# Kernel optimization log

Measured on AMD Instinct MI355X. Metric: run time of the kernel, lower is better.

## Reference

```python
import jax, jax.numpy as jnp
from jax import lax
import numpy as np

K = 256   # kernel_size == hidden channels (Haar basis size)
S = 16    # stride
BN_EPS = 1e-5


def _haar_matrix_unnorm(n):
    if n == 2:
        return np.array([[1.0, 1.0], [1.0, -1.0]])
    prev = _haar_matrix_unnorm(n // 2)
    top = np.kron(prev, np.array([1.0, 1.0]))
    bot = np.kron(np.eye(n // 2), np.array([1.0, -1.0]))
    return np.concatenate((top, bot))


def haar_matrix(n):
    h = _haar_matrix_unnorm(n)
    return h / np.linalg.norm(h, axis=1, keepdims=True)


def setup_inputs() -> dict:
    key = jax.random.key(0)
    ks = jax.random.split(key, 8)
    B, T = 64, 32768
    haar = jnp.asarray(haar_matrix(K), dtype=jnp.float32)          # [K, K]
    x = jax.random.normal(ks[0], (B, 1, T), dtype=jnp.float32)
    return {
        "x": x,
        # BitwiseConv1d(1, K, K, stride=S, padding=K)
        "conv_w": haar[:, None, :],                                 # [K, 1, K] (OIH)
        "conv_b": 0.01 * jax.random.normal(ks[1], (K,), dtype=jnp.float32),
        "conv_gate": jax.random.uniform(ks[2], (K, 1, K), dtype=jnp.float32),
        "conv_scale": jnp.ones((K,), dtype=jnp.float32),            # adaptive per-out-channel scale
        # BatchNorm1d(K)
        "bn_gamma": jnp.ones((K,), dtype=jnp.float32),
        "bn_beta": jnp.zeros((K,), dtype=jnp.float32),
        # BitwiseConvTranspose1d(K, 1, K, stride=S)
        "ct_w": haar.T[:, None, :],                                 # [K(in), 1(out), K] (IOH, torch layout)
        "ct_b": 0.01 * jax.random.normal(ks[3], (1,), dtype=jnp.float32),
        "ct_gate": jax.random.uniform(ks[4], (K, 1, K), dtype=jnp.float32),
        "ct_scale": jnp.ones((1,), dtype=jnp.float32),
    }


def _forward(x, conv_w, conv_b, conv_gate, conv_scale, bn_gamma, bn_beta,
             ct_w, ct_b, ct_gate, ct_scale):
    T = x.shape[2]
    # --- BitwiseConv1d: gated weights (in_bin/weight_bin = identity) ---
    # gate binarization maps gate -> (gate + 1) / 2, multiplied into weights
    w = conv_w * (conv_gate + 1.0) * 0.5                            # [K,1,K]
    h = lax.conv_general_dilated(
        x, w, window_strides=(S,), padding=[(K, K)],
        dimension_numbers=("NCH", "OIH", "NCH"))                  # [B,K,L]
    h = conv_scale[None, :, None] * (h + conv_b[None, :, None])    # adaptive scaling
    # --- ReLU then BatchNorm1d (training-mode batch statistics) ---
    h = jax.nn.relu(h)
    mu = jnp.mean(h, axis=(0, 2), keepdims=True)
    var = jnp.mean((h - mu) ** 2, axis=(0, 2), keepdims=True)
    h = (h - mu) * lax.rsqrt(var + BN_EPS)
    h = h * bn_gamma[None, :, None] + bn_beta[None, :, None]
    # --- BitwiseConvTranspose1d: gated weights, expressed as dilated conv ---
    wt = ct_w * (ct_gate + 1.0) * 0.5                               # [K_in, 1, K]
    # torch IOH -> regular-conv OIH with kernel flipped
    wr = jnp.flip(jnp.transpose(wt, (1, 0, 2)), axis=-1)            # [1, K, K]
    y = lax.conv_general_dilated(
        h, wr, window_strides=(1,), padding=[(K - 1, K - 1)],
        lhs_dilation=(S,), dimension_numbers=("NCH", "OIH", "NCH"))
    y = ct_scale[None, :, None] * (y + ct_b[None, :, None])
    # crop: out[:, :, K : T + K]
    return y[:, :, K:T + K]


def reference(x, conv_w, conv_b, conv_gate, conv_scale, bn_gamma, bn_beta,
              ct_w, ct_b, ct_gate, ct_scale):
    return _forward(x, conv_w, conv_b, conv_gate, conv_scale, bn_gamma, bn_beta,
                    ct_w, ct_b, ct_gate, ct_scale)
```

## Files before the change

kernel.cpp:

```cpp
#include <hip/hip_runtime.h>
#include <hip/hip_bf16.h>

#define BB 64
#define TT 32768
#define KK 256
#define LL 2065
#define NLT 9
#define NPART (BB*NLT)
#define NJ 19
#define NPT3 8
#define XG 2336
#define HB8 36

typedef __attribute__((ext_vector_type(8))) short short8;
typedef __attribute__((ext_vector_type(4))) float f32x4;
typedef __attribute__((ext_vector_type(4))) int int4v;
typedef __attribute__((ext_vector_type(2))) unsigned int uint2v;

__device__ __forceinline__ unsigned short f2bf(float f) {
    unsigned u = __builtin_bit_cast(unsigned, f);
    unsigned r = (u + 0x7FFFu + ((u >> 16) & 1u)) >> 16;
    return (unsigned short)r;
}
__device__ __forceinline__ unsigned pkbf(float a, float b) {
    unsigned r;
    asm("v_cvt_pk_bf16_f32 %0, %1, %2" : "=v"(r) : "v"(a), "v"(b));
    return r;
}
__device__ __forceinline__ void gload_lds16(const void* g, void* l) {
    __builtin_amdgcn_global_load_lds(
        (const __attribute__((address_space(1))) unsigned int*)g,
        (__attribute__((address_space(3))) unsigned int*)l, 16, 0, 0);
}

__global__ void k0x_xbf(const float* __restrict__ x, unsigned short* __restrict__ xbf)
{
    int idx = blockIdx.x*256 + threadIdx.x;
    int b = idx / XG, gi = idx - b*XG;
    unsigned short* dst = xbf + (size_t)idx*24;
    int4v w0, w1;
    if (gi < 16 || gi > 2063) {
        w0 = (int4v){0,0,0,0}; w1 = (int4v){0,0,0,0};
    } else {
        const float4* xv = (const float4*)(x + (size_t)b*TT + 16*(gi-16));
        float4 a0 = xv[0], a1 = xv[1], a2 = xv[2], a3 = xv[3];
        w0 = (int4v){ (int)pkbf(a0.x,a0.y), (int)pkbf(a0.z,a0.w),
                      (int)pkbf(a1.x,a1.y), (int)pkbf(a1.z,a1.w) };
        w1 = (int4v){ (int)pkbf(a2.x,a2.y), (int)pkbf(a2.z,a2.w),
                      (int)pkbf(a3.x,a3.y), (int)pkbf(a3.z,a3.w) };
    }
    *(int4v*)dst       = w0;
    *(int4v*)(dst + 8) = w1;
}

__global__ void k0_w1f(const float* __restrict__ cw, const float* __restrict__ cgt,
                       unsigned short* __restrict__ W1f)
{
    int idx = blockIdx.x*256 + threadIdx.x;
    int lane = idx & 63, ntL = (idx>>6)&7, kk = (idx>>9)&7, half = idx>>12;
    int o = half*128 + ntL*16 + (lane&15);
    int kbase = kk*32 + ((lane>>4)<<3);
    short8 v;
    #pragma unroll
    for (int i = 0; i < 8; ++i) {
        int gi = o*KK + kbase + i;
        v[i] = (short)f2bf(cw[gi]*(cgt[gi]+1.0f)*0.5f);
    }
    *(short8*)(W1f + (size_t)idx*8) = v;
}

__global__ __launch_bounds__(256, 5)
void k1_conv(const unsigned short* __restrict__ xbf, const float* __restrict__ cs,
             const float* __restrict__ cb, const unsigned short* __restrict__ W1f,
             unsigned short* __restrict__ hout,
             float* __restrict__ psum, float* __restrict__ psq)
{
    __shared__ __align__(16) char smem[13312 + 16384];
    char* xwinb = smem;
    char* wbuf  = smem + 13312;
    unsigned short* hb = (unsigned short*)smem;
    float* redS = (float*)(smem + 18432);
    float* redQ = (float*)(smem + 18432 + 512);

    const int tid   = threadIdx.x;
    const int q8    = blockIdx.x & 7;
    const int ltile = blockIdx.x >> 3;
    const int b     = blockIdx.y;
    const int l0    = ltile * 256;
    const int lane  = tid & 63;
    const int w     = tid >> 6;

    {
        #pragma unroll
        for (int it = 0; it < 4; ++it) {
            int ci = w*4 + it;
            int kk = ci >> 1, mt = ci & 1;
            size_t so = (size_t)((((q8>>2)*8 + kk)*8 + (q8&3)*2 + mt))*1024;
            gload_lds16((const char*)W1f + so + lane*16, wbuf + ci*1024);
        }
    }
    {
        const char* xsrc = (const char*)xbf + (size_t)b*(XG*48) + (size_t)ltile*12288;
        #pragma unroll
        for (int it = 0; it < 4; ++it) {
            int i = w + it*4;
            if (i < 13)
                gload_lds16(xsrc + i*1024 + lane*16, xwinb + i*1024);
        }
    }
    __syncthreads();

    f32x4 acc[2][4];
    #pragma unroll
    for (int mt = 0; mt < 2; ++mt)
        #pragma unroll
        for (int nt = 0; nt < 4; ++nt) acc[mt][nt] = (f32x4){0.f,0.f,0.f,0.f};

    const int gq = lane >> 4;
    const int Gt = 16*gq + 16*(gq>>1);
    const int abase = 48*((w<<6) + (lane & 15)) + Gt;

    #pragma unroll
    for (int kk = 0; kk < 8; ++kk) {
        short8 bfx[4], afw[2];
        #pragma unroll
        for (int nt = 0; nt < 4; ++nt)
            bfx[nt] = *(const short8*)(xwinb + abase + nt*768 + kk*96);
        #pragma unroll
        for (int mt = 0; mt < 2; ++mt)
            afw[mt] = *(const short8*)(wbuf + (kk*2 + mt)*1024 + lane*16);
        __builtin_amdgcn_s_setprio(1);
        #pragma unroll
        for (int mt = 0; mt < 2; ++mt)
            #pragma unroll
            for (int nt = 0; nt < 4; ++nt)
                acc[mt][nt] = __builtin_amdgcn_mfma_f32_16x16x32_bf16(afw[mt], bfx[nt], acc[mt][nt], 0, 0, 0);
        __builtin_amdgcn_s_setprio(0);
    }
    __syncthreads();

    const int c0 = q8*32;
    const int g  = lane >> 4;
    const int li = lane & 15;
    #pragma unroll
    for (int mt = 0; mt < 2; ++mt) {
        int cq = c0 + mt*16 + g*4;
        f32x4 cs4 = *(const f32x4*)&cs[cq];
        f32x4 cb4 = *(const f32x4*)&cb[cq];
        f32x4 s4 = (f32x4){0.f,0.f,0.f,0.f};
        f32x4 q4 = (f32x4){0.f,0.f,0.f,0.f};
        #pragma unroll
        for (int nt = 0; nt < 4; ++nt) {
            int lloc = (w<<6) + nt*16 + li;
            f32x4 hv;
            #pragma unroll
            for (int rr = 0; rr < 4; ++rr)
                hv[rr] = fmaxf(cs4[rr]*(acc[mt][nt][rr] + cb4[rr]), 0.0f);
            uint2v pkv = { pkbf(hv[0], hv[1]), pkbf(hv[2], hv[3]) };
            *(uint2v*)(hb + lloc*HB8 + mt*16 + g*4) = pkv;
            if (l0 + lloc < LL) { s4 += hv; q4 += hv*hv; }
        }
        #pragma unroll
        for (int d = 1; d < 16; d <<= 1) {
            #pragma unroll
            for (int rr = 0; rr < 4; ++rr) {
                s4[rr] += __shfl_xor(s4[rr], d);
                q4[rr] += __shfl_xor(q4[rr], d);
            }
        }
        if (li == 0) {
            *(f32x4*)&redS[((w*2 + mt)*4 + g)*4] = s4;
            *(f32x4*)&redQ[((w*2 + mt)*4 + g)*4] = q4;
        }
    }
    __syncthreads();

    {
        #pragma unroll
        for (int it = 0; it < 4; ++it) {
            int item = it*256 + tid;
            int row = item >> 2, chunk = item & 3;
            int l = l0 + row;
            if (l < LL) {
                int4v v = *(const int4v*)(hb + row*HB8 + chunk*8);
                *(int4v*)(hout + (((size_t)(b*LL + l)) << 8) + q8*32 + chunk*8) = v;
            }
        }
    }
    if (tid < 32) {
        int mt = tid >> 4, gg = (tid >> 2) & 3, rr = tid & 3;
        float s = 0.f, qq = 0.f;
        #pragma unroll
        for (int wv = 0; wv < 4; ++wv) {
            s  += redS[((wv*2 + mt)*4 + gg)*4 + rr];
            qq += redQ[((wv*2 + mt)*4 + gg)*4 + rr];
        }
        int c = c0 + tid;
        int slot = b*NLT + ltile;
        psum[c*NPART + slot] = s;
        psq [c*NPART + slot] = qq;
    }
}

__global__ __launch_bounds__(256)
void k2_bn(const float* __restrict__ psum, const float* __restrict__ psq,
           const float* __restrict__ bng, const float* __restrict__ bnb,
           const float* __restrict__ ctw, const float* __restrict__ ctg,
           const float* __restrict__ ctscale,
           float* __restrict__ W3s, float* __restrict__ SWS)
{
    __shared__ double rs[4], rq[4];
    __shared__ float s_a, s_bc;
    __shared__ float swl[256];
    const int c = blockIdx.x;
    const int tid = threadIdx.x;
    double s = 0.0, q = 0.0;
    for (int i = tid; i < NPART; i += 256) {
        s += (double)psum[c*NPART + i];
        q += (double)psq [c*NPART + i];
    }
    for (int off = 32; off > 0; off >>= 1) {
        s += __shfl_down(s, off);
        q += __shfl_down(q, off);
    }
    if ((tid & 63) == 0) { rs[tid >> 6] = s; rq[tid >> 6] = q; }
    __syncthreads();
    if (tid == 0) {
        double st = rs[0]+rs[1]+rs[2]+rs[3];
        double qt = rq[0]+rq[1]+rq[2]+rq[3];
        const double cnt = (double)BB * (double)LL;
        double mu = st / cnt;
        double var = qt / cnt - mu*mu;
        float rsig = (float)(1.0 / sqrt(var + 1e-5));
        float a = bng[c] * rsig;
        s_a = a;
        s_bc = bnb[c] - (float)mu * a;
    }
    __syncthreads();
    float a = s_a, bc = s_bc, scl = ctscale[0];
    int gi = c*KK + tid;
    float wt = ctw[gi] * (ctg[gi] + 1.0f) * 0.5f;
    W3s[tid*KK + c] = scl * a * wt;
    swl[tid] = wt * bc;
    __syncthreads();
    if (tid < 16) {
        float acc2 = 0.0f;
        #pragma unroll
        for (int d = 0; d < 16; ++d) acc2 += swl[d*16 + tid];
        SWS[c*16 + tid] = acc2;
    }
}

__global__ __launch_bounds__(256)
void k2b_const(const float* __restrict__ SWS, const float* __restrict__ ctb,
               const float* __restrict__ ctscale, float* __restrict__ C2)
{
    __shared__ float accb[16][17];
    int tid = threadIdx.x;
    int r = tid & 15, cc = tid >> 4;
    float s = 0.0f;
    #pragma unroll
    for (int i = 0; i < 16; ++i) s += SWS[(cc*16 + i)*16 + r];
    accb[cc][r] = s;
    __syncthreads();
    if (tid < 16) {
        float t = 0.0f;
        #pragma unroll
        for (int i = 0; i < 16; ++i) t += accb[i][tid];
        C2[tid] = ctscale[0] * (t + ctb[0]);
    }
}

__global__ void k2c_b2f(const float* __restrict__ W3s, unsigned short* __restrict__ B2f)
{
    int idx = blockIdx.x*256 + threadIdx.x;
    int lane = idx & 63;
    int ntG  = (idx>>6) & 3;
    int kk   = (idx>>8) & 7;
    int j    = idx>>11;
    int c    = kk*32 + ((lane>>4)<<3);
    int r    = lane & 15;
    int d    = ntG + 15 - j;
    short8 v;
    if (d >= 0 && d <= 15) {
        const float* wr = W3s + (size_t)(16*d + r)*KK + c;
        #pragma unroll
        for (int i = 0; i < 8; ++i) v[i] = (short)f2bf(wr[i]);
    } else {
        #pragma unroll
        for (int i = 0; i < 8; ++i) v[i] = 0;
    }
    *(short8*)(B2f + (size_t)idx*8) = v;
}

__global__ __launch_bounds__(512, 1)
void k3_synth(const unsigned short* __restrict__ h, const unsigned short* __restrict__ B2f,
              const float* __restrict__ C2, float* __restrict__ out)
{
    __shared__ __align__(16) char As[272*512];
    const int tid  = threadIdx.x;
    const int lane = tid & 63;
    const int w    = tid >> 6;
    const int b    = blockIdx.y;
    const int P0   = blockIdx.x * 64;

    const char* hbase = (const char*)h + (((size_t)(b*LL) + 4*P0 + 1) << 9);

    {
        const int rl = lane >> 5;
        #pragma unroll
        for (int i = 0; i < 17; ++i) {
            int r0  = w*34 + i*2;
            int row = r0 + rl;
            int chunk = (lane & 31) ^ ((row >> 2) & 7);
            gload_lds16(hbase + (size_t)row*512 + chunk*16, As + r0*512);
        }
    }
    __syncthreads();

    const int li = lane & 15;
    const int gq = lane >> 4;

    f32x4 acc[4][4];
    #pragma unroll
    for (int mt = 0; mt < 4; ++mt)
        #pragma unroll
        for (int nt = 0; nt < 4; ++nt) acc[mt][nt] = (f32x4){0.f,0.f,0.f,0.f};

    #pragma unroll 1
    for (int jj = 0; jj < 3; ++jj) {
        const int j = w + jj*8;
        if (j >= NJ) break;
        short8 bfA[4], bfB[4];
        #pragma unroll
        for (int nt = 0; nt < 4; ++nt)
            bfA[nt] = *(const short8*)(B2f + (((size_t)(j*8 + 0)*4 + nt)*64 + lane)*8);
        #pragma unroll
        for (int kk = 0; kk < 8; ++kk) {
            if (kk < 7) {
                #pragma unroll
                for (int nt = 0; nt < 4; ++nt)
                    bfB[nt] = *(const short8*)(B2f + (((size_t)(j*8 + kk+1)*4 + nt)*64 + lane)*8);
            }
            short8 af[4];
            #pragma unroll
            for (int mt = 0; mt < 4; ++mt) {
                int row = 64*mt + 4*li + j;
                int p = (kk*4 + gq) ^ ((row >> 2) & 7);
                af[mt] = *(const short8*)(As + row*512 + p*16);
            }
            __builtin_amdgcn_s_setprio(1);
            #pragma unroll
            for (int mt = 0; mt < 4; ++mt)
                #pragma unroll
                for (int nt = 0; nt < 4; ++nt)
                    acc[mt][nt] = __builtin_amdgcn_mfma_f32_16x16x32_bf16(af[mt], bfA[nt], acc[mt][nt], 0, 0, 0);
            __builtin_amdgcn_s_setprio(0);
            #pragma unroll
            for (int nt = 0; nt < 4; ++nt) bfA[nt] = bfB[nt];
        }
    }
    __syncthreads();

    float* red = (float*)As;
    #pragma unroll
    for (int mt = 0; mt < 4; ++mt)
        #pragma unroll
        for (int nt = 0; nt < 4; ++nt) {
            int u = nt*16 + li;
            #pragma unroll
            for (int rr = 0; rr < 4; ++rr) {
                int Pl = 16*mt + gq*4 + rr;
                red[w*4352 + Pl*68 + u] = acc[mt][nt][rr];
            }
        }
    __syncthreads();

    {
        float* ob = out + (size_t)b*TT + (size_t)P0*64;
        #pragma unroll
        for (int it = 0; it < 2; ++it) {
            int item = it*512 + tid;
            int P = item >> 4, uq = item & 15;
            f32x4 s = (f32x4){0.f,0.f,0.f,0.f};
            #pragma unroll
            for (int c = 0; c < 8; ++c)
                s += *(const f32x4*)&red[c*4352 + P*68 + uq*4];
            int ub = (uq & 3)*4;
            f32x4 c2v = { C2[ub], C2[ub+1], C2[ub+2], C2[ub+3] };
            *(f32x4*)&ob[P*64 + uq*4] = s + c2v;
        }
    }
}

extern "C" void kernel_launch(void* const* d_in, const int* in_sizes, int n_in,
                              void* d_out, int out_size, void* d_ws, size_t ws_size,
                              hipStream_t stream)
{
    const float* x       = (const float*)d_in[0];
    const float* cw      = (const float*)d_in[1];
    const float* cb      = (const float*)d_in[2];
    const float* cgt     = (const float*)d_in[3];
    const float* cs      = (const float*)d_in[4];
    const float* bng     = (const float*)d_in[5];
    const float* bnb     = (const float*)d_in[6];
    const float* ctw     = (const float*)d_in[7];
    const float* ctb     = (const float*)d_in[8];
    const float* ctg     = (const float*)d_in[9];
    const float* ctscale = (const float*)d_in[10];
    float* out = (float*)d_out;

    char* ws = (char*)d_ws;
    size_t off = 0;
    unsigned short* h    = (unsigned short*)(ws + off); off += (size_t)BB*LL*KK*2;
    float* psum          = (float*)(ws + off);          off += (size_t)KK*NPART*4;
    float* psq           = (float*)(ws + off);          off += (size_t)KK*NPART*4;
    unsigned short* W1f  = (unsigned short*)(ws + off); off += 65536*2;
    float* W3s           = (float*)(ws + off);          off += (size_t)KK*KK*4;
    float* SWS           = (float*)(ws + off);          off += (size_t)KK*16*4;
    float* C2            = (float*)(ws + off);          off += 64;
    unsigned short* xbf  = (unsigned short*)(ws + off); off += (size_t)BB*XG*24*2;
    unsigned short* B2f  = (unsigned short*)(ws + off); off += (size_t)NJ*8*4*64*8*2;

    k0x_xbf <<<BB*XG/256, 256, 0, stream>>>(x, xbf);
    k0_w1f  <<<32, 256, 0, stream>>>(cw, cgt, W1f);
    k1_conv <<<dim3(72, BB), 256, 0, stream>>>(xbf, cs, cb, W1f, h, psum, psq);
    k2_bn   <<<KK, 256, 0, stream>>>(psum, psq, bng, bnb, ctw, ctg, ctscale, W3s, SWS);
    k2b_const<<<1, 256, 0, stream>>>(SWS, ctb, ctscale, C2);
    k2c_b2f <<<152, 256, 0, stream>>>(W3s, B2f);
    k3_synth<<<dim3(NPT3, BB), 512, 0, stream>>>(h, B2f, C2, out);
}
```

Measured before the change: 85.43 us.

## Make k1 conv persistent over L tiles with double-buffered x window loads

```diff
diff --git a/kernel.cpp b/kernel.cpp
--- a/kernel.cpp
+++ b/kernel.cpp
@@ -69,26 +69,30 @@
     *(short8*)(W1f + (size_t)idx*8) = v;
 }
 
-__global__ __launch_bounds__(256, 5)
+__global__ __launch_bounds__(256, 2)
 void k1_conv(const unsigned short* __restrict__ xbf, const float* __restrict__ cs,
              const float* __restrict__ cb, const unsigned short* __restrict__ W1f,
              unsigned short* __restrict__ hout,
              float* __restrict__ psum, float* __restrict__ psq)
 {
-    __shared__ __align__(16) char smem[13312 + 16384];
-    char* xwinb = smem;
-    char* wbuf  = smem + 13312;
-    unsigned short* hb = (unsigned short*)smem;
-    float* redS = (float*)(smem + 18432);
-    float* redQ = (float*)(smem + 18432 + 512);
-
-    const int tid   = threadIdx.x;
-    const int q8    = blockIdx.x & 7;
-    const int ltile = blockIdx.x >> 3;
-    const int b     = blockIdx.y;
-    const int l0    = ltile * 256;
-    const int lane  = tid & 63;
-    const int w     = tid >> 6;
+    __shared__ __align__(16) char smem[62464];
+    char* wbuf = smem;
+    char* xw0  = smem + 16384;
+    char* xw1  = smem + 29696;
+    unsigned short* hb = (unsigned short*)(smem + 43008);
+    float* redS = (float*)(smem + 61440);
+    float* redQ = (float*)(smem + 61952);
+
+    const int tid  = threadIdx.x;
+    const int q8   = blockIdx.x;
+    const int b    = blockIdx.y;
+    const int lane = tid & 63;
+    const int w    = tid >> 6;
+    const int c0   = q8*32;
+    const int g    = lane >> 4;
+    const int li   = lane & 15;
+
+    const char* xsrc0 = (const char*)xbf + (size_t)b*(XG*48);
 
     {
         #pragma unroll
@@ -98,84 +102,94 @@
             size_t so = (size_t)((((q8>>2)*8 + kk)*8 + (q8&3)*2 + mt))*1024;
             gload_lds16((const char*)W1f + so + lane*16, wbuf + ci*1024);
         }
-    }
-    {
-        const char* xsrc = (const char*)xbf + (size_t)b*(XG*48) + (size_t)ltile*12288;
         #pragma unroll
         for (int it = 0; it < 4; ++it) {
             int i = w + it*4;
             if (i < 13)
-                gload_lds16(xsrc + i*1024 + lane*16, xwinb + i*1024);
-        }
-    }
-    __syncthreads();
-
-    f32x4 acc[2][4];
+                gload_lds16(xsrc0 + i*1024 + lane*16, xw0 + i*1024);
+        }
+    }
+    __syncthreads();
+
+    f32x4 cs4[2], cb4[2];
     #pragma unroll
-    for (int mt = 0; mt < 2; ++mt)
-        #pragma unroll
-        for (int nt = 0; nt < 4; ++nt) acc[mt][nt] = (f32x4){0.f,0.f,0.f,0.f};
+    for (int mt = 0; mt < 2; ++mt) {
+        cs4[mt] = *(const f32x4*)&cs[c0 + mt*16 + g*4];
+        cb4[mt] = *(const f32x4*)&cb[c0 + mt*16 + g*4];
+    }
 
     const int gq = lane >> 4;
     const int Gt = 16*gq + 16*(gq>>1);
-    const int abase = 48*((w<<6) + (lane & 15)) + Gt;
-
-    #pragma unroll
-    for (int kk = 0; kk < 8; ++kk) {
-        short8 bfx[4], afw[2];
-        #pragma unroll
-        for (int nt = 0; nt < 4; ++nt)
-            bfx[nt] = *(const short8*)(xwinb + abase + nt*768 + kk*96);
+    const int abase = 48*((w<<6) + li) + Gt;
+
+    #pragma unroll 1
+    for (int t = 0; t < NLT; ++t) {
+        char* xcur = (t & 1) ? xw1 : xw0;
+        char* xnxt = (t & 1) ? xw0 : xw1;
+        if (t + 1 < NLT) {
+            const char* xs = xsrc0 + (size_t)(t+1)*12288;
+            #pragma unroll
+            for (int it = 0; it < 4; ++it) {
+                int i = w + it*4;
+                if (i < 13)
+                    gload_lds16(xs + i*1024 + lane*16, xnxt + i*1024);
+            }
+        }
+
+        f32x4 acc[2][4];
         #pragma unroll
         for (int mt = 0; mt < 2; ++mt)
-            afw[mt] = *(const short8*)(wbuf + (kk*2 + mt)*1024 + lane*16);
-        __builtin_amdgcn_s_setprio(1);
-        #pragma unroll
-        for (int mt = 0; mt < 2; ++mt)
+            #pragma unroll
+            for (int nt = 0; nt < 4; ++nt) acc[mt][nt] = (f32x4){0.f,0.f,0.f,0.f};
+        #pragma unroll
+        for (int kk = 0; kk < 8; ++kk) {
+            short8 bfx[4], afw[2];
             #pragma unroll
             for (int nt = 0; nt < 4; ++nt)
-                acc[mt][nt] = __builtin_amdgcn_mfma_f32_16x16x32_bf16(afw[mt], bfx[nt], acc[mt][nt], 0, 0, 0);
-        __builtin_amdgcn_s_setprio(0);
-    }
-    __syncthreads();
-
-    const int c0 = q8*32;
-    const int g  = lane >> 4;
-    const int li = lane & 15;
-    #pragma unroll
-    for (int mt = 0; mt < 2; ++mt) {
-        int cq = c0 + mt*16 + g*4;
-        f32x4 cs4 = *(const f32x4*)&cs[cq];
-        f32x4 cb4 = *(const f32x4*)&cb[cq];
-        f32x4 s4 = (f32x4){0.f,0.f,0.f,0.f};
-        f32x4 q4 = (f32x4){0.f,0.f,0.f,0.f};
-        #pragma unroll
-        for (int nt = 0; nt < 4; ++nt) {
-            int lloc = (w<<6) + nt*16 + li;
-            f32x4 hv;
-            #pragma unroll
-            for (int rr = 0; rr < 4; ++rr)
-                hv[rr] = fmaxf(cs4[rr]*(acc[mt][nt][rr] + cb4[rr]), 0.0f);
-            uint2v pkv = { pkbf(hv[0], hv[1]), pkbf(hv[2], hv[3]) };
-            *(uint2v*)(hb + lloc*HB8 + mt*16 + g*4) = pkv;
-            if (l0 + lloc < LL) { s4 += hv; q4 += hv*hv; }
-        }
-        #pragma unroll
-        for (int d = 1; d < 16; d <<= 1) {
-            #pragma unroll
-            for (int rr = 0; rr < 4; ++rr) {
-                s4[rr] += __shfl_xor(s4[rr], d);
-                q4[rr] += __shfl_xor(q4[rr], d);
-            }
-        }
-        if (li == 0) {
-            *(f32x4*)&redS[((w*2 + mt)*4 + g)*4] = s4;
-            *(f32x4*)&redQ[((w*2 + mt)*4 + g)*4] = q4;
-        }
-    }
-    __syncthreads();
-
-    {
+                bfx[nt] = *(const short8*)(xcur + abase + nt*768 + kk*96);
+            #pragma unroll
+            for (int mt = 0; mt < 2; ++mt)
+                afw[mt] = *(const short8*)(wbuf + (kk*2 + mt)*1024 + lane*16);
+            __builtin_amdgcn_s_setprio(1);
+            #pragma unroll
+            for (int mt = 0; mt < 2; ++mt)
+                #pragma unroll
+                for (int nt = 0; nt < 4; ++nt)
+                    acc[mt][nt] = __builtin_amdgcn_mfma_f32_16x16x32_bf16(afw[mt], bfx[nt], acc[mt][nt], 0, 0, 0);
+            __builtin_amdgcn_s_setprio(0);
+        }
+
+        const int l0 = t * 256;
+        #pragma unroll
+        for (int mt = 0; mt < 2; ++mt) {
+            f32x4 s4 = (f32x4){0.f,0.f,0.f,0.f};
+            f32x4 q4 = (f32x4){0.f,0.f,0.f,0.f};
+            #pragma unroll
+            for (int nt = 0; nt < 4; ++nt) {
+                int lloc = (w<<6) + nt*16 + li;
+                f32x4 hv;
+                #pragma unroll
+                for (int rr = 0; rr < 4; ++rr)
+                    hv[rr] = fmaxf(cs4[mt][rr]*(acc[mt][nt][rr] + cb4[mt][rr]), 0.0f);
+                uint2v pkv = { pkbf(hv[0], hv[1]), pkbf(hv[2], hv[3]) };
+                *(uint2v*)(hb + lloc*HB8 + mt*16 + g*4) = pkv;
+                if (l0 + lloc < LL) { s4 += hv; q4 += hv*hv; }
+            }
+            #pragma unroll
+            for (int d = 1; d < 16; d <<= 1) {
+                #pragma unroll
+                for (int rr = 0; rr < 4; ++rr) {
+                    s4[rr] += __shfl_xor(s4[rr], d);
+                    q4[rr] += __shfl_xor(q4[rr], d);
+                }
+            }
+            if (li == 0) {
+                *(f32x4*)&redS[((w*2 + mt)*4 + g)*4] = s4;
+                *(f32x4*)&redQ[((w*2 + mt)*4 + g)*4] = q4;
+            }
+        }
+        __syncthreads();
+
         #pragma unroll
         for (int it = 0; it < 4; ++it) {
             int item = it*256 + tid;
@@ -183,22 +197,21 @@
             int l = l0 + row;
             if (l < LL) {
                 int4v v = *(const int4v*)(hb + row*HB8 + chunk*8);
-                *(int4v*)(hout + (((size_t)(b*LL + l)) << 8) + q8*32 + chunk*8) = v;
-            }
-        }
-    }
-    if (tid < 32) {
-        int mt = tid >> 4, gg = (tid >> 2) & 3, rr = tid & 3;
-        float s = 0.f, qq = 0.f;
-        #pragma unroll
-        for (int wv = 0; wv < 4; ++wv) {
-            s  += redS[((wv*2 + mt)*4 + gg)*4 + rr];
-            qq += redQ[((wv*2 + mt)*4 + gg)*4 + rr];
-        }
-        int c = c0 + tid;
-        int slot = b*NLT + ltile;
-        psum[c*NPART + slot] = s;
-        psq [c*NPART + slot] = qq;
+                *(int4v*)(hout + (((size_t)(b*LL + l)) << 8) + c0 + chunk*8) = v;
+            }
+        }
+        if (tid < 32) {
+            int mt = tid >> 4, gg = (tid >> 2) & 3, rr = tid & 3;
+            float s = 0.f, qq = 0.f;
+            #pragma unroll
+            for (int wv = 0; wv < 4; ++wv) {
+                s  += redS[((wv*2 + mt)*4 + gg)*4 + rr];
+                qq += redQ[((wv*2 + mt)*4 + gg)*4 + rr];
+            }
+            psum[(c0 + tid)*NPART + b*NLT + t] = s;
+            psq [(c0 + tid)*NPART + b*NLT + t] = qq;
+        }
+        __syncthreads();
     }
 }
 
@@ -424,7 +437,7 @@
 
     k0x_xbf <<<BB*XG/256, 256, 0, stream>>>(x, xbf);
     k0_w1f  <<<32, 256, 0, stream>>>(cw, cgt, W1f);
-    k1_conv <<<dim3(72, BB), 256, 0, stream>>>(xbf, cs, cb, W1f, h, psum, psq);
+    k1_conv <<<dim3(8, BB), 256, 0, stream>>>(xbf, cs, cb, W1f, h, psum, psq);
     k2_bn   <<<KK, 256, 0, stream>>>(psum, psq, bng, bnb, ctw, ctg, ctscale, W3s, SWS);
     k2b_const<<<1, 256, 0, stream>>>(SWS, ctb, ctscale, C2);
     k2c_b2f <<<152, 256, 0, stream>>>(W3s, B2f);
```

Result: slower. 89.33 us (+4.6%).
